# Optimization experiments

Measured on AMD Instinct MI355X. Metric: run time of the kernel, lower is better.

Reference implementation:

```python
import jax, jax.numpy as jnp
import numpy as np

B, N, NT = 64, 1024, 100
DIM, KD, NH, D = 256, 16, 8, 64
DH = D * NH            # 512
NH_KD = KD * NH        # 128
H_KV = DH + NH_KD      # 640
PROJ_IN = DH + 1000    # 1512
NUM_OFFSETS = 10000    # 100x100 grid of (|dx|,|dy|)
EPS = 1e-5


def _bn_params(key, n):
    k1, k2, k3, k4 = jax.random.split(key, 4)
    gamma = 1.0 + 0.1 * jax.random.normal(k1, (n,), jnp.float32)
    beta = 0.1 * jax.random.normal(k2, (n,), jnp.float32)
    mean = 0.1 * jax.random.normal(k3, (n,), jnp.float32)
    var = 0.5 + jax.random.uniform(k4, (n,), jnp.float32)
    return gamma, beta, mean, var


def setup_inputs() -> dict:
    key = jax.random.key(0)
    ks = jax.random.split(key, 9)
    x = jax.random.normal(ks[0], (B, N, DIM), jnp.float32)
    text = jax.random.normal(ks[1], (NT, DIM), jnp.float32)
    kv_w = jax.random.normal(ks[2], (H_KV, DIM), jnp.float32) * (DIM ** -0.5)
    q_w = jax.random.normal(ks[3], (NH_KD, DIM), jnp.float32) * (DIM ** -0.5)
    proj_w = jax.random.normal(ks[4], (DIM, PROJ_IN), jnp.float32) * (PROJ_IN ** -0.5)
    kv_g, kv_b, kv_m, kv_v = _bn_params(ks[5], H_KV)
    q_g, q_b, q_m, q_v = _bn_params(ks[6], NH_KD)
    proj_g, proj_b, proj_m, proj_v = _bn_params(ks[7], DIM)
    biases = 0.02 * jax.random.normal(ks[8], (NH, NUM_OFFSETS), jnp.float32)
    return {
        'x': x, 'text': text,
        'kv_w': kv_w, 'kv_g': kv_g, 'kv_b': kv_b, 'kv_m': kv_m, 'kv_v': kv_v,
        'q_w': q_w, 'q_g': q_g, 'q_b': q_b, 'q_m': q_m, 'q_v': q_v,
        'proj_w': proj_w, 'proj_g': proj_g, 'proj_b': proj_b, 'proj_m': proj_m, 'proj_v': proj_v,
        'biases': biases, 'H': 32, 'W': 32,
    }


def _linear_bn(x, w, g, b, m, v):
    # Linear (no bias) followed by BatchNorm1d in eval mode, per feature.
    y = x @ w.T
    return (y - m) * (g * jax.lax.rsqrt(v + EPS)) + b


def _hardswish(x):
    return x * jnp.clip(x + 3.0, 0.0, 6.0) * (1.0 / 6.0)


def _bias_idx(nt, h, w):
    # text tokens laid on (row, col) grid of width 100; image tokens on HxW grid.
    t = jnp.arange(nt)
    p1x, p1y = t // 100, t % 100
    n = jnp.arange(h * w)
    p2x, p2y = n // w, n % w
    # offset id = |dx| * 100 + |dy| (first-appearance order of the offset dict)
    return jnp.abs(p1x[:, None] - p2x[None, :]) * 100 + jnp.abs(p1y[:, None] - p2y[None, :])


def reference(x, text, kv_w, kv_g, kv_b, kv_m, kv_v,
              q_w, q_g, q_b, q_m, q_v,
              proj_w, proj_g, proj_b, proj_m, proj_v,
              biases, H, W):
    b, n, _ = x.shape
    nt = text.shape[0]
    scale = KD ** -0.5

    kv = _linear_bn(x, kv_w, kv_g, kv_b, kv_m, kv_v).reshape(b, n, NH, KD + D)
    k = kv[..., :KD]                 # [B, N, NH, KD]
    v = kv[..., KD:]                 # [B, N, NH, D]
    q = _linear_bn(text, q_w, q_g, q_b, q_m, q_v).reshape(nt, NH, KD)  # [NT, NH, KD]

    idx = _bias_idx(nt, H, W)        # [NT, N] int32
    attn = jnp.einsum('thd,bnhd->bhtn', q, k) * scale + biases[:, idx]  # [B, NH, NT, N]
    attn = jax.nn.softmax(attn, axis=-1)

    v_flat = v.reshape(b, n, DH)                                    # [B, N, DH]
    attn_feat = attn.reshape(b, NH * nt, n).transpose(0, 2, 1)      # [B, N, NH*NT]
    comp = jnp.zeros((b, n, 1000 - nt * NH), x.dtype)
    v_cat = jnp.concatenate([v_flat, attn_feat, comp], axis=-1)     # [B, N, DH+1000]

    return _linear_bn(_hardswish(v_cat), proj_w, proj_g, proj_b, proj_m, proj_v)
```

## Files before the change

### kernel.cpp

```cpp
#include <hip/hip_runtime.h>
#include <hip/hip_bf16.h>

#define B_    64
#define N_    1024
#define NT_   100
#define DIM_  256
#define KD_   16
#define NH_   8
#define D_    64
#define DH_   512
#define HKV_  640
#define PROJIN_ 1512
#define KCAT_ 1312
#define EPS_  1e-5f
#define M_    (B_*N_)

typedef __attribute__((ext_vector_type(8))) short bf16x8;
typedef __attribute__((ext_vector_type(4))) float f32x4;

__device__ __forceinline__ float bf_lo(unsigned int p){ union{unsigned int i;float f;}c; c.i=p<<16; return c.f; }
__device__ __forceinline__ float bf_hi(unsigned int p){ union{unsigned int i;float f;}c; c.i=p&0xffff0000u; return c.f; }
__device__ __forceinline__ int iabs(int x){ return x<0?-x:x; }
__device__ __forceinline__ unsigned short bfr(float f){ __hip_bfloat16 h=__float2bfloat16(f); return *(unsigned short*)&h; }
__device__ __forceinline__ float bfl(unsigned short u){ union{unsigned int i;float f;}c; c.i=(unsigned int)u<<16; return c.f; }

#define GLDS16(src, dst) __builtin_amdgcn_global_load_lds( \
    (const __attribute__((address_space(1))) void*)(src),  \
    (__attribute__((address_space(3))) void*)(dst), 16, 0, 0)

__global__ __launch_bounds__(256) void p0_cvt(
    const float* __restrict__ x, const float* __restrict__ kvw, const float* __restrict__ pw,
    unsigned short* __restrict__ xb, unsigned short* __restrict__ kvwb, unsigned short* __restrict__ pwb)
{
    const size_t stride = (size_t)gridDim.x * 256;
    const size_t i0 = (size_t)blockIdx.x * 256 + threadIdx.x;
    for (size_t q = i0; q < (size_t)M_*DIM_/4; q += stride) {
        float4 v = ((const float4*)x)[q];
        ushort4 o; o.x=bfr(v.x); o.y=bfr(v.y); o.z=bfr(v.z); o.w=bfr(v.w);
        ((ushort4*)xb)[q] = o;
    }
    for (size_t q = i0; q < (size_t)HKV_*DIM_/4; q += stride) {
        float4 v = ((const float4*)kvw)[q];
        ushort4 o; o.x=bfr(v.x); o.y=bfr(v.y); o.z=bfr(v.z); o.w=bfr(v.w);
        ((ushort4*)kvwb)[q] = o;
    }
    for (size_t q = i0; q < (size_t)DIM_*KCAT_/4; q += stride) {
        const int row = (int)(q / (KCAT_/4)), cq = (int)(q % (KCAT_/4));
        float4 v = ((const float4*)(pw + (size_t)row*PROJIN_))[cq];
        ushort4 o; o.x=bfr(v.x); o.y=bfr(v.y); o.z=bfr(v.z); o.w=bfr(v.w);
        ((ushort4*)pwb)[q] = o;
    }
}

__global__ __launch_bounds__(256,2) void k1g(
    const unsigned short* __restrict__ xb, const unsigned short* __restrict__ wb,
    const float* __restrict__ g, const float* __restrict__ bb,
    const float* __restrict__ mn, const float* __restrict__ vr,
    unsigned short* __restrict__ outC)
{
    __shared__ unsigned short As[128*32];
    __shared__ unsigned short Bs[128*32];
    const int tid = threadIdx.x;
    const int wave = tid >> 6, lane = tid & 63;
    const int m0 = blockIdx.y * 128, n0 = blockIdx.x * 128;
    const int wm = (wave >> 1) * 64, wn = (wave & 1) * 64;
    const int srow = lane >> 2, scol = (lane & 3) * 8;
    f32x4 acc[4][4];
    #pragma unroll
    for (int i=0;i<4;i++)
        #pragma unroll
        for (int j=0;j<4;j++) acc[i][j] = (f32x4){0.f,0.f,0.f,0.f};

    for (int k0 = 0; k0 < DIM_; k0 += 32) {
        #pragma unroll
        for (int i = 0; i < 2; i++) {
            const int rr = (wave*2 + i)*16 + srow;
            GLDS16(xb + (size_t)(m0+rr)*DIM_ + k0 + scol, As + (wave*2+i)*512);
            GLDS16(wb + (size_t)(n0+rr)*DIM_ + k0 + scol, Bs + (wave*2+i)*512);
        }
        __syncthreads();
        bf16x8 af[4], bfv[4];
        #pragma unroll
        for (int f = 0; f < 4; f++) {
            af[f]  = *(const bf16x8*)&As[(wm + f*16 + (lane&15))*32 + (lane>>4)*8];
            bfv[f] = *(const bf16x8*)&Bs[(wn + f*16 + (lane&15))*32 + (lane>>4)*8];
        }
        #pragma unroll
        for (int fi = 0; fi < 4; fi++)
            #pragma unroll
            for (int fj = 0; fj < 4; fj++)
                acc[fi][fj] = __builtin_amdgcn_mfma_f32_16x16x32_bf16(af[fi], bfv[fj], acc[fi][fj], 0,0,0);
        __syncthreads();
    }
    #pragma unroll
    for (int fj = 0; fj < 4; fj++) {
        const int col = n0 + wn + fj*16 + (lane & 15);
        const float s = g[col] * rsqrtf(vr[col] + EPS_);
        const float o = bb[col] - mn[col] * s;
        const bool vcol = (col - (col/80)*80) >= 16;
        #pragma unroll
        for (int fi = 0; fi < 4; fi++)
            #pragma unroll
            for (int r = 0; r < 4; r++) {
                const int m = m0 + wm + fi*16 + (lane>>4)*4 + r;
                float v = acc[fi][fj][r] * s + o;
                if (vcol) v = v * fminf(fmaxf(v + 3.f, 0.f), 6.f) * (1.f/6.f);
                outC[(size_t)m * HKV_ + col] = bfr(v);
            }
    }
}

__global__ __launch_bounds__(128) void k2_q(
    const float* __restrict__ text, const float* __restrict__ q_w,
    const float* __restrict__ g, const float* __restrict__ bb,
    const float* __restrict__ mn, const float* __restrict__ vr,
    float* __restrict__ q_out)
{
    __shared__ float ts[DIM_];
    const int t = blockIdx.x, j = threadIdx.x;
    for (int i = threadIdx.x; i < DIM_; i += 128) ts[i] = text[t * DIM_ + i];
    __syncthreads();
    float acc = 0.f;
    for (int k = 0; k < DIM_; k++) acc += ts[k] * q_w[j * DIM_ + k];
    const float s = g[j] * rsqrtf(vr[j] + EPS_);
    q_out[t * 128 + j] = acc * s + (bb[j] - mn[j] * s);
}

__global__ __launch_bounds__(256) void k3a(
    const unsigned short* __restrict__ kvf, const float* __restrict__ qb,
    const float* __restrict__ biases, const int* __restrict__ Wp,
    float* __restrict__ wsinv)
{
    __shared__ unsigned short Kl[N_*16];
    __shared__ unsigned short Ql[112*32];
    __shared__ unsigned short bsl[3200];
    const int bh = blockIdx.x, b = bh >> 3, h = bh & 7;
    const int tid = threadIdx.x;
    const int wave = tid >> 6, lane = tid & 63;
    const int w = *Wp;

    #pragma unroll
    for (int i = 0; i < 8; i++) {
        const int C = i*256 + tid;
        const int n = C >> 1, half = C & 1;
        GLDS16(kvf + (size_t)(b*N_ + n)*HKV_ + h*80 + half*8, Kl + (i*256 + wave*64)*8);
    }
    for (int i = tid; i < 112*32; i += 256) {
        const int t = i >> 5, d = i & 31;
        Ql[i] = (t < NT_ && d < 16) ? bfr(qb[t*128 + h*16 + d]) : (unsigned short)0;
    }
    for (int i = tid; i < 3200; i += 256) bsl[i] = bfr(biases[h*10000 + i]);
    __syncthreads();

    const int kg = lane >> 4;
    for (int tt = wave; tt < 7; tt += 4) {
        bf16x8 qf = *(const bf16x8*)&Ql[(tt*16 + (lane&15))*32 + kg*8];
        float rs[4] = {0.f,0.f,0.f,0.f};
        const int tb = tt*16 + ((lane>>4)<<2);
        for (int nt = 0; nt < 64; nt++) {
            const int n = nt*16 + (lane & 15);
            bf16x8 kf = *(const bf16x8*)&Kl[n*16 + (kg&1)*8];
            f32x4 a = __builtin_amdgcn_mfma_f32_16x16x32_bf16(qf, kf, (f32x4){0.f,0.f,0.f,0.f}, 0,0,0);
            const int px = n / w;
            const int py = n - px*w;
            const int pxm = px*100;
            #pragma unroll
            for (int r = 0; r < 4; r++) {
                int dy = iabs(tb + r - py); dy = dy > 99 ? 99 : dy;
                rs[r] += __expf(fmaf(a[r], 0.25f, bfl(bsl[pxm + dy])));
            }
        }
        #pragma unroll
        for (int r = 0; r < 4; r++) {
            #pragma unroll
            for (int msk = 1; msk < 16; msk <<= 1) rs[r] += __shfl_xor(rs[r], msk);
        }
        if ((lane & 15) == 0) {
            #pragma unroll
            for (int r = 0; r < 4; r++)
                wsinv[(size_t)bh*112 + tb + r] = 1.0f / rs[r];
        }
    }
}

__global__ __launch_bounds__(256) void k3b(
    const unsigned short* __restrict__ kvf, const float* __restrict__ qb,
    const float* __restrict__ biases, const int* __restrict__ Wp,
    const float* __restrict__ wsinv, unsigned short* __restrict__ attn_t)
{
    __shared__ unsigned short Kl[128*128];
    __shared__ unsigned short Ql[112*128];
    __shared__ unsigned short bsl[4000];
    __shared__ float invs[800];
    __shared__ unsigned short zbuf[8];
    const int bx = blockIdx.x, b = bx >> 3, n0 = (bx & 7) * 128;
    const int tid = threadIdx.x;
    const int wave = tid >> 6, lane = tid & 63;
    const int w = *Wp;
    const int pxlo = n0 / w;

    if (tid < 8) zbuf[tid] = 0;
    #pragma unroll
    for (int i = 0; i < 8; i++) {
        const int C = i*256 + tid;
        const int n = C >> 4, gslot = C & 15;
        const int h2g = gslot ^ (n & 7);
        GLDS16(kvf + (size_t)(b*N_ + n0 + n)*HKV_ + (h2g>>1)*80 + (h2g&1)*8,
               Kl + (i*256 + wave*64)*8);
    }
    for (int G = tid; G < 1792; G += 256) {
        const int t = G >> 4, dg = G & 15;
        ushort4 o0 = {0,0,0,0}, o1 = {0,0,0,0};
        if (t < NT_) {
            const float* src = qb + t*128 + dg*8;
            float4 v0 = *(const float4*)src, v1 = *(const float4*)(src+4);
            o0.x=bfr(v0.x); o0.y=bfr(v0.y); o0.z=bfr(v0.z); o0.w=bfr(v0.w);
            o1.x=bfr(v1.x); o1.y=bfr(v1.y); o1.z=bfr(v1.z); o1.w=bfr(v1.w);
        }
        unsigned short* dst = &Ql[t*128 + (dg ^ (t & 7))*8];
        *(ushort4*)dst = o0; *(ushort4*)(dst+4) = o1;
    }
    for (int i = tid; i < 4000; i += 256) {
        const int pr = i / 800, rem = i - pr*800;
        const int h = rem / 100, dy = rem - h*100;
        int row = pxlo + pr; row = row > 99 ? 99 : row;
        bsl[i] = bfr(biases[h*10000 + row*100 + dy]);
    }
    for (int i = tid; i < 800; i += 256) {
        const int h = i / 100, t = i - h*100;
        invs[i] = wsinv[(size_t)(b*8 + h)*112 + t];
    }
    __syncthreads();

    const int kg = lane >> 4;
    const int l7 = lane & 7;
    for (int nn = wave; nn < 8; nn += 4) {
        const int ngb = n0 + nn*16 + ((lane>>4)<<2);
        int prx[4], pyv[4];
        #pragma unroll
        for (int r = 0; r < 4; r++) {
            const int ng = ngb + r;
            const int px = ng / w;
            prx[r] = px - pxlo;
            pyv[r] = ng - px*w;
        }
        const int t = (lane & 15);
        for (int h = 0; h < 8; h++) {
            const int nloc = nn*16 + (lane & 15);
            const unsigned short* aptr = (kg < 2)
                ? &Kl[nloc*128 + ((((h<<1)|kg) ^ l7))*8] : zbuf;
            bf16x8 kf = *(const bf16x8*)aptr;
            for (int tt = 0; tt < 7; tt++) {
                const int tc = tt*16 + t;
                bf16x8 qf = *(const bf16x8*)&Ql[tc*128 + ((((h<<1)|(kg&1)) ^ l7))*8];
                f32x4 a = __builtin_amdgcn_mfma_f32_16x16x32_bf16(kf, qf, (f32x4){0.f,0.f,0.f,0.f}, 0,0,0);
                const int tcl = tc > 99 ? 99 : tc;
                const float invv = invs[h*100 + tcl];
                if (tc < NT_) {
                    #pragma unroll
                    for (int r = 0; r < 4; r++) {
                        int dy = iabs(tc - pyv[r]); dy = dy > 99 ? 99 : dy;
                        const float bb = bfl(bsl[(prx[r]*8 + h)*100 + dy]);
                        const float e = __expf(fmaf(a[r], 0.25f, bb));
                        const float p = e * invv;
                        const float hs = p * (p + 3.f) * (1.f/6.f);
                        attn_t[(size_t)(b*N_ + ngb + r)*800 + h*100 + tc] = bfr(hs);
                    }
                }
            }
        }
    }
}

__global__ __launch_bounds__(512,2) void k4g(
    const unsigned short* __restrict__ kvf, const unsigned short* __restrict__ attn_t,
    const unsigned short* __restrict__ pwb,
    const float* __restrict__ g, const float* __restrict__ bb,
    const float* __restrict__ mn, const float* __restrict__ vr,
    float* __restrict__ out)
{
    __shared__ unsigned short As[128*32];
    __shared__ unsigned short Bs[256*32];
    const int tid = threadIdx.x;
    const int wave = tid >> 6, lane = tid & 63;
    const int m0 = blockIdx.x * 128;
    const int wm = (wave >> 2) * 64, wn = (wave & 3) * 64;
    const int arow = tid >> 2, ac8 = (tid & 3) * 8;
    f32x4 acc[4][4];
    #pragma unroll
    for (int i=0;i<4;i++)
        #pragma unroll
        for (int j=0;j<4;j++) acc[i][j] = (f32x4){0.f,0.f,0.f,0.f};

    for (int ks = 0; ks < KCAT_/32; ks++) {
        const int k0 = ks * 32;
        {
            const size_t mrow = (size_t)(m0 + arow);
            const unsigned short* src;
            if (k0 < DH_) {
                const int h = k0 >> 6;
                src = kvf + mrow*HKV_ + h*80 + 16 + (k0 & 32) + ac8;
            } else {
                src = attn_t + mrow*800 + (k0 - DH_) + ac8;
            }
            GLDS16(src, As + wave*512);
        }
        #pragma unroll
        for (int i = 0; i < 2; i++) {
            const int C = i*512 + tid;
            const int row = C >> 2, c8 = (C & 3)*8;
            GLDS16(pwb + (size_t)row*KCAT_ + k0 + c8, Bs + (i*512 + wave*64)*8);
        }
        __syncthreads();
        bf16x8 af[4], bfv[4];
        #pragma unroll
        for (int f = 0; f < 4; f++) {
            af[f]  = *(const bf16x8*)&As[(wm + f*16 + (lane&15))*32 + (lane>>4)*8];
            bfv[f] = *(const bf16x8*)&Bs[(wn + f*16 + (lane&15))*32 + (lane>>4)*8];
        }
        #pragma unroll
        for (int fi = 0; fi < 4; fi++)
            #pragma unroll
            for (int fj = 0; fj < 4; fj++)
                acc[fi][fj] = __builtin_amdgcn_mfma_f32_16x16x32_bf16(af[fi], bfv[fj], acc[fi][fj], 0,0,0);
        __syncthreads();
    }
    #pragma unroll
    for (int fj = 0; fj < 4; fj++) {
        const int col = wn + fj*16 + (lane & 15);
        const float s = g[col] * rsqrtf(vr[col] + EPS_);
        const float o = bb[col] - mn[col] * s;
        #pragma unroll
        for (int fi = 0; fi < 4; fi++)
            #pragma unroll
            for (int r = 0; r < 4; r++) {
                const int m = m0 + wm + fi*16 + (lane>>4)*4 + r;
                out[(size_t)m * DIM_ + col] = acc[fi][fj][r] * s + o;
            }
    }
}

extern "C" void kernel_launch(void* const* d_in, const int* in_sizes, int n_in,
                              void* d_out, int out_size, void* d_ws, size_t ws_size,
                              hipStream_t stream) {
    const float* x      = (const float*)d_in[0];
    const float* text   = (const float*)d_in[1];
    const float* kv_w   = (const float*)d_in[2];
    const float* kv_g   = (const float*)d_in[3];
    const float* kv_b   = (const float*)d_in[4];
    const float* kv_m   = (const float*)d_in[5];
    const float* kv_v   = (const float*)d_in[6];
    const float* q_w    = (const float*)d_in[7];
    const float* q_g    = (const float*)d_in[8];
    const float* q_b    = (const float*)d_in[9];
    const float* q_m    = (const float*)d_in[10];
    const float* q_v    = (const float*)d_in[11];
    const float* proj_w = (const float*)d_in[12];
    const float* proj_g = (const float*)d_in[13];
    const float* proj_b = (const float*)d_in[14];
    const float* proj_m = (const float*)d_in[15];
    const float* proj_v = (const float*)d_in[16];
    const float* biases = (const float*)d_in[17];
    const int*   Wp     = (const int*)d_in[19];
    float* out = (float*)d_out;

    char* w = (char*)d_ws;
    size_t off = 0;
    auto alloc = [&](size_t bytes) { void* p = w + off; off += (bytes + 255) & ~255ull; return p; };
    unsigned short* xb    = (unsigned short*)alloc((size_t)M_*DIM_*2);
    unsigned short* kvwb  = (unsigned short*)alloc((size_t)HKV_*DIM_*2);
    unsigned short* pwb   = (unsigned short*)alloc((size_t)DIM_*KCAT_*2);
    unsigned short* kvbuf = (unsigned short*)alloc((size_t)M_*HKV_*2);
    unsigned short* attnt = (unsigned short*)alloc((size_t)M_*800*2);
    float*          qbuf  = (float*)alloc((size_t)NT_*128*4);
    float*          wsinv = (float*)alloc((size_t)B_*NH_*112*4);

    p0_cvt<<<2048, 256, 0, stream>>>(x, kv_w, proj_w, xb, kvwb, pwb);
    k1g<<<dim3(HKV_/128, M_/128), 256, 0, stream>>>(xb, kvwb, kv_g, kv_b, kv_m, kv_v, kvbuf);
    k2_q<<<NT_, 128, 0, stream>>>(text, q_w, q_g, q_b, q_m, q_v, qbuf);
    k3a<<<B_*NH_, 256, 0, stream>>>(kvbuf, qbuf, biases, Wp, wsinv);
    k3b<<<B_*NH_, 256, 0, stream>>>(kvbuf, qbuf, biases, Wp, wsinv, attnt);
    k4g<<<M_/128, 512, 0, stream>>>(kvbuf, attnt, pwb, proj_g, proj_b, proj_m, proj_v, out);
}
```

Baseline: 374.9 us.

## Fuse x bf16 conversion into KV GEMM, split K/V buffers, coalesce stores

Drops the separate fp32-to-bf16 pass over x and converts x tiles inside the KV GEMM's LDS staging. The GEMM epilogue is staged through LDS so it writes 16-byte coalesced rows into separate contiguous K and V buffers. The GEMM grid is remapped into a swizzled 1D order, and the attention-probability kernel now stores four packed bf16 values per write. This removes one full read/write pass over x and the strided scalar stores, at the cost of synchronous global loads for A in the GEMM main loop and extra LDS use.

```diff
diff --git a/kernel.cpp b/kernel.cpp
--- a/kernel.cpp
+++ b/kernel.cpp
@@ -18,8 +18,6 @@
 typedef __attribute__((ext_vector_type(8))) short bf16x8;
 typedef __attribute__((ext_vector_type(4))) float f32x4;
 
-__device__ __forceinline__ float bf_lo(unsigned int p){ union{unsigned int i;float f;}c; c.i=p<<16; return c.f; }
-__device__ __forceinline__ float bf_hi(unsigned int p){ union{unsigned int i;float f;}c; c.i=p&0xffff0000u; return c.f; }
 __device__ __forceinline__ int iabs(int x){ return x<0?-x:x; }
 __device__ __forceinline__ unsigned short bfr(float f){ __hip_bfloat16 h=__float2bfloat16(f); return *(unsigned short*)&h; }
 __device__ __forceinline__ float bfl(unsigned short u){ union{unsigned int i;float f;}c; c.i=(unsigned int)u<<16; return c.f; }
@@ -29,16 +27,11 @@
     (__attribute__((address_space(3))) void*)(dst), 16, 0, 0)
 
 __global__ __launch_bounds__(256) void p0_cvt(
-    const float* __restrict__ x, const float* __restrict__ kvw, const float* __restrict__ pw,
-    unsigned short* __restrict__ xb, unsigned short* __restrict__ kvwb, unsigned short* __restrict__ pwb)
+    const float* __restrict__ kvw, const float* __restrict__ pw,
+    unsigned short* __restrict__ kvwb, unsigned short* __restrict__ pwb)
 {
     const size_t stride = (size_t)gridDim.x * 256;
     const size_t i0 = (size_t)blockIdx.x * 256 + threadIdx.x;
-    for (size_t q = i0; q < (size_t)M_*DIM_/4; q += stride) {
-        float4 v = ((const float4*)x)[q];
-        ushort4 o; o.x=bfr(v.x); o.y=bfr(v.y); o.z=bfr(v.z); o.w=bfr(v.w);
-        ((ushort4*)xb)[q] = o;
-    }
     for (size_t q = i0; q < (size_t)HKV_*DIM_/4; q += stride) {
         float4 v = ((const float4*)kvw)[q];
         ushort4 o; o.x=bfr(v.x); o.y=bfr(v.y); o.z=bfr(v.z); o.w=bfr(v.w);
@@ -53,18 +46,22 @@
 }
 
 __global__ __launch_bounds__(256,2) void k1g(
-    const unsigned short* __restrict__ xb, const unsigned short* __restrict__ wb,
+    const float* __restrict__ x, const unsigned short* __restrict__ wb,
     const float* __restrict__ g, const float* __restrict__ bb,
     const float* __restrict__ mn, const float* __restrict__ vr,
-    unsigned short* __restrict__ outC)
+    unsigned short* __restrict__ kb, unsigned short* __restrict__ vb)
 {
     __shared__ unsigned short As[128*32];
     __shared__ unsigned short Bs[128*32];
+    __shared__ unsigned short Ls[64*128];
     const int tid = threadIdx.x;
     const int wave = tid >> 6, lane = tid & 63;
-    const int m0 = blockIdx.y * 128, n0 = blockIdx.x * 128;
+    const int logical = (blockIdx.x & 7) * 320 + (blockIdx.x >> 3);
+    const int nblk = logical % 5, mblk = logical / 5;
+    const int m0 = mblk * 128, n0 = nblk * 128;
     const int wm = (wave >> 1) * 64, wn = (wave & 1) * 64;
     const int srow = lane >> 2, scol = (lane & 3) * 8;
+    const int sr = tid >> 1, sh = (tid & 1) * 16;
     f32x4 acc[4][4];
     #pragma unroll
     for (int i=0;i<4;i++)
@@ -75,8 +72,21 @@
         #pragma unroll
         for (int i = 0; i < 2; i++) {
             const int rr = (wave*2 + i)*16 + srow;
-            GLDS16(xb + (size_t)(m0+rr)*DIM_ + k0 + scol, As + (wave*2+i)*512);
             GLDS16(wb + (size_t)(n0+rr)*DIM_ + k0 + scol, Bs + (wave*2+i)*512);
+        }
+        {
+            const float* xs = x + (size_t)(m0+sr)*DIM_ + k0 + sh;
+            float4 v0 = ((const float4*)xs)[0], v1 = ((const float4*)xs)[1];
+            float4 v2 = ((const float4*)xs)[2], v3 = ((const float4*)xs)[3];
+            ushort4 a0, a1, b0, b1;
+            a0.x=bfr(v0.x); a0.y=bfr(v0.y); a0.z=bfr(v0.z); a0.w=bfr(v0.w);
+            a1.x=bfr(v1.x); a1.y=bfr(v1.y); a1.z=bfr(v1.z); a1.w=bfr(v1.w);
+            b0.x=bfr(v2.x); b0.y=bfr(v2.y); b0.z=bfr(v2.z); b0.w=bfr(v2.w);
+            b1.x=bfr(v3.x); b1.y=bfr(v3.y); b1.z=bfr(v3.z); b1.w=bfr(v3.w);
+            *(ushort4*)&As[sr*32 + sh]      = a0;
+            *(ushort4*)&As[sr*32 + sh + 4]  = a1;
+            *(ushort4*)&As[sr*32 + sh + 8]  = b0;
+            *(ushort4*)&As[sr*32 + sh + 12] = b1;
         }
         __syncthreads();
         bf16x8 af[4], bfv[4];
@@ -92,21 +102,42 @@
                 acc[fi][fj] = __builtin_amdgcn_mfma_f32_16x16x32_bf16(af[fi], bfv[fj], acc[fi][fj], 0,0,0);
         __syncthreads();
     }
-    #pragma unroll
-    for (int fj = 0; fj < 4; fj++) {
-        const int col = n0 + wn + fj*16 + (lane & 15);
-        const float s = g[col] * rsqrtf(vr[col] + EPS_);
-        const float o = bb[col] - mn[col] * s;
-        const bool vcol = (col - (col/80)*80) >= 16;
-        #pragma unroll
-        for (int fi = 0; fi < 4; fi++)
-            #pragma unroll
-            for (int r = 0; r < 4; r++) {
-                const int m = m0 + wm + fi*16 + (lane>>4)*4 + r;
-                float v = acc[fi][fj][r] * s + o;
-                if (vcol) v = v * fminf(fmaxf(v + 3.f, 0.f), 6.f) * (1.f/6.f);
-                outC[(size_t)m * HKV_ + col] = bfr(v);
+
+    #pragma unroll
+    for (int pass = 0; pass < 2; ++pass) {
+        if ((wave >> 1) == pass) {
+            #pragma unroll
+            for (int fj = 0; fj < 4; fj++) {
+                const int col = wn + fj*16 + (lane & 15);
+                const int gcol = n0 + col;
+                const float s = g[gcol] * rsqrtf(vr[gcol] + EPS_);
+                const float o = bb[gcol] - mn[gcol] * s;
+                const bool vcol = (gcol - (gcol/80)*80) >= 16;
+                #pragma unroll
+                for (int fi = 0; fi < 4; fi++)
+                    #pragma unroll
+                    for (int r = 0; r < 4; r++) {
+                        float v = acc[fi][fj][r] * s + o;
+                        if (vcol) v = v * fminf(fmaxf(v + 3.f, 0.f), 6.f) * (1.f/6.f);
+                        Ls[(fi*16 + (lane>>4)*4 + r)*128 + col] = bfr(v);
+                    }
             }
+        }
+        __syncthreads();
+        #pragma unroll
+        for (int it = 0; it < 4; ++it) {
+            const int row = it*16 + (tid >> 4);
+            const int c8  = tid & 15;
+            bf16x8 val = *(const bf16x8*)&Ls[row*128 + c8*8];
+            const int gcol = n0 + c8*8;
+            const int h = gcol / 80, rem = gcol - h*80;
+            const int m = m0 + pass*64 + row;
+            unsigned short* dst = (rem < 16)
+                ? (kb + (size_t)m*128 + h*16 + rem)
+                : (vb + (size_t)m*512 + h*64 + (rem - 16));
+            *(bf16x8*)dst = val;
+        }
+        __syncthreads();
     }
 }
 
@@ -127,7 +158,7 @@
 }
 
 __global__ __launch_bounds__(256) void k3a(
-    const unsigned short* __restrict__ kvf, const float* __restrict__ qb,
+    const unsigned short* __restrict__ kb, const float* __restrict__ qb,
     const float* __restrict__ biases, const int* __restrict__ Wp,
     float* __restrict__ wsinv)
 {
@@ -143,7 +174,7 @@
     for (int i = 0; i < 8; i++) {
         const int C = i*256 + tid;
         const int n = C >> 1, half = C & 1;
-        GLDS16(kvf + (size_t)(b*N_ + n)*HKV_ + h*80 + half*8, Kl + (i*256 + wave*64)*8);
+        GLDS16(kb + (size_t)(b*N_ + n)*128 + h*16 + half*8, Kl + (i*256 + wave*64)*8);
     }
     for (int i = tid; i < 112*32; i += 256) {
         const int t = i >> 5, d = i & 31;
@@ -184,7 +215,7 @@
 }
 
 __global__ __launch_bounds__(256) void k3b(
-    const unsigned short* __restrict__ kvf, const float* __restrict__ qb,
+    const unsigned short* __restrict__ kb, const float* __restrict__ qb,
     const float* __restrict__ biases, const int* __restrict__ Wp,
     const float* __restrict__ wsinv, unsigned short* __restrict__ attn_t)
 {
@@ -205,8 +236,7 @@
         const int C = i*256 + tid;
         const int n = C >> 4, gslot = C & 15;
         const int h2g = gslot ^ (n & 7);
-        GLDS16(kvf + (size_t)(b*N_ + n0 + n)*HKV_ + (h2g>>1)*80 + (h2g&1)*8,
-               Kl + (i*256 + wave*64)*8);
+        GLDS16(kb + (size_t)(b*N_ + n0 + n)*128 + h2g*8, Kl + (i*256 + wave*64)*8);
     }
     for (int G = tid; G < 1792; G += 256) {
         const int t = G >> 4, dg = G & 15;
@@ -233,39 +263,38 @@
     __syncthreads();
 
     const int kg = lane >> 4;
-    const int l7 = lane & 7;
-    for (int nn = wave; nn < 8; nn += 4) {
-        const int ngb = n0 + nn*16 + ((lane>>4)<<2);
-        int prx[4], pyv[4];
-        #pragma unroll
-        for (int r = 0; r < 4; r++) {
-            const int ng = ngb + r;
-            const int px = ng / w;
-            prx[r] = px - pxlo;
-            pyv[r] = ng - px*w;
-        }
-        const int t = (lane & 15);
+    const int l15 = lane & 15, l7 = lane & 7;
+    #pragma unroll
+    for (int nn2 = 0; nn2 < 2; nn2++) {
+        const int nn = wave + nn2*4;
+        const int ng = n0 + nn*16 + l15;
+        const int px = ng / w;
+        const int prx = px - pxlo, py = ng - px*w;
+        const size_t obase = (size_t)(b*N_ + ng)*800;
+        const int nloc = nn*16 + l15;
         for (int h = 0; h < 8; h++) {
-            const int nloc = nn*16 + (lane & 15);
-            const unsigned short* aptr = (kg < 2)
-                ? &Kl[nloc*128 + ((((h<<1)|kg) ^ l7))*8] : zbuf;
-            bf16x8 kf = *(const bf16x8*)aptr;
+            const int h2 = h*2;
+            bf16x8 kf = *(const bf16x8*)&Kl[nloc*128 + ((h2 | (kg&1)) ^ l7)*8];
             for (int tt = 0; tt < 7; tt++) {
-                const int tc = tt*16 + t;
-                bf16x8 qf = *(const bf16x8*)&Ql[tc*128 + ((((h<<1)|(kg&1)) ^ l7))*8];
-                f32x4 a = __builtin_amdgcn_mfma_f32_16x16x32_bf16(kf, qf, (f32x4){0.f,0.f,0.f,0.f}, 0,0,0);
-                const int tcl = tc > 99 ? 99 : tc;
-                const float invv = invs[h*100 + tcl];
-                if (tc < NT_) {
+                const int trow = tt*16 + l15;
+                const unsigned short* aptr = (kg < 2)
+                    ? &Ql[trow*128 + (((h2 | kg) ^ l7))*8] : zbuf;
+                bf16x8 qf = *(const bf16x8*)aptr;
+                f32x4 a = __builtin_amdgcn_mfma_f32_16x16x32_bf16(qf, kf, (f32x4){0.f,0.f,0.f,0.f}, 0,0,0);
+                const int tb0 = tt*16 + (kg << 2);
+                if (tb0 < NT_) {
+                    ushort4 pk;
+                    unsigned short* pkp = (unsigned short*)&pk;
                     #pragma unroll
                     for (int r = 0; r < 4; r++) {
-                        int dy = iabs(tc - pyv[r]); dy = dy > 99 ? 99 : dy;
-                        const float bb = bfl(bsl[(prx[r]*8 + h)*100 + dy]);
-                        const float e = __expf(fmaf(a[r], 0.25f, bb));
-                        const float p = e * invv;
-                        const float hs = p * (p + 3.f) * (1.f/6.f);
-                        attn_t[(size_t)(b*N_ + ngb + r)*800 + h*100 + tc] = bfr(hs);
+                        const int t = tb0 + r;
+                        int dy = iabs(t - py); dy = dy > 99 ? 99 : dy;
+                        const float bbv = bfl(bsl[(prx*8 + h)*100 + dy]);
+                        const float e = __expf(fmaf(a[r], 0.25f, bbv));
+                        const float p = e * invs[h*100 + t];
+                        pkp[r] = bfr(p * (p + 3.f) * (1.f/6.f));
                     }
+                    *(ushort4*)(attn_t + obase + h*100 + tb0) = pk;
                 }
             }
         }
@@ -273,7 +302,7 @@
 }
 
 __global__ __launch_bounds__(512,2) void k4g(
-    const unsigned short* __restrict__ kvf, const unsigned short* __restrict__ attn_t,
+    const unsigned short* __restrict__ vb, const unsigned short* __restrict__ attn_t,
     const unsigned short* __restrict__ pwb,
     const float* __restrict__ g, const float* __restrict__ bb,
     const float* __restrict__ mn, const float* __restrict__ vr,
@@ -296,13 +325,9 @@
         const int k0 = ks * 32;
         {
             const size_t mrow = (size_t)(m0 + arow);
-            const unsigned short* src;
-            if (k0 < DH_) {
-                const int h = k0 >> 6;
-                src = kvf + mrow*HKV_ + h*80 + 16 + (k0 & 32) + ac8;
-            } else {
-                src = attn_t + mrow*800 + (k0 - DH_) + ac8;
-            }
+            const unsigned short* src = (k0 < DH_)
+                ? (vb + mrow*512 + k0 + ac8)
+                : (attn_t + mrow*800 + (k0 - DH_) + ac8);
             GLDS16(src, As + wave*512);
         }
         #pragma unroll
@@ -367,18 +392,18 @@
     char* w = (char*)d_ws;
     size_t off = 0;
     auto alloc = [&](size_t bytes) { void* p = w + off; off += (bytes + 255) & ~255ull; return p; };
-    unsigned short* xb    = (unsigned short*)alloc((size_t)M_*DIM_*2);
     unsigned short* kvwb  = (unsigned short*)alloc((size_t)HKV_*DIM_*2);
     unsigned short* pwb   = (unsigned short*)alloc((size_t)DIM_*KCAT_*2);
-    unsigned short* kvbuf = (unsigned short*)alloc((size_t)M_*HKV_*2);
+    unsigned short* kbuf  = (unsigned short*)alloc((size_t)M_*128*2);
+    unsigned short* vbuf  = (unsigned short*)alloc((size_t)M_*512*2);
     unsigned short* attnt = (unsigned short*)alloc((size_t)M_*800*2);
     float*          qbuf  = (float*)alloc((size_t)NT_*128*4);
     float*          wsinv = (float*)alloc((size_t)B_*NH_*112*4);
 
-    p0_cvt<<<2048, 256, 0, stream>>>(x, kv_w, proj_w, xb, kvwb, pwb);
-    k1g<<<dim3(HKV_/128, M_/128), 256, 0, stream>>>(xb, kvwb, kv_g, kv_b, kv_m, kv_v, kvbuf);
+    p0_cvt<<<256, 256, 0, stream>>>(kv_w, proj_w, kvwb, pwb);
+    k1g<<<2560, 256, 0, stream>>>(x, kvwb, kv_g, kv_b, kv_m, kv_v, kbuf, vbuf);
     k2_q<<<NT_, 128, 0, stream>>>(text, q_w, q_g, q_b, q_m, q_v, qbuf);
-    k3a<<<B_*NH_, 256, 0, stream>>>(kvbuf, qbuf, biases, Wp, wsinv);
-    k3b<<<B_*NH_, 256, 0, stream>>>(kvbuf, qbuf, biases, Wp, wsinv, attnt);
-    k4g<<<M_/128, 512, 0, stream>>>(kvbuf, attnt, pwb, proj_g, proj_b, proj_m, proj_v, out);
-}
+    k3a<<<B_*NH_, 256, 0, stream>>>(kbuf, qbuf, biases, Wp, wsinv);
+    k3b<<<B_*NH_, 256, 0, stream>>>(kbuf, qbuf, biases, Wp, wsinv, attnt);
+    k4g<<<M_/128, 512, 0, stream>>>(vbuf, attnt, pwb, proj_g, proj_b, proj_m, proj_v, out);
+}
```

New measurement: 371.8 us. Within noise of the previous version (-0.8%).
